# Performance work log

Measured on AMD Instinct MI355X. Metric: run time of the kernel, lower is better.

The kernel has to match this reference:

```python
import jax, jax.numpy as jnp
import numpy as np

B, C, H, W = 32, 256, 56, 56
HEADS, M, EXP = 8, 7, 4


def _rel_pos_index(m):
    # Swin V1 pair-wise relative position index, [m*m, m*m] (static)
    coords = np.stack(np.meshgrid(np.arange(m), np.arange(m), indexing='ij'))  # [2,m,m]
    cf = coords.reshape(2, -1)
    rel = (cf[:, :, None] - cf[:, None, :]).transpose(1, 2, 0).copy()
    rel[:, :, 0] += m - 1
    rel[:, :, 1] += m - 1
    rel[:, :, 0] *= 2 * m - 1
    return jnp.asarray(rel.sum(-1))


def setup_inputs():
    key = jax.random.key(0)
    ks = jax.random.split(key, 8)
    s = lambda k, shp: jax.random.normal(k, shp, jnp.float32) * 0.02
    return {
        'x': jax.random.normal(ks[0], (B, C, H, W), jnp.float32),
        'qkv_w': s(ks[1], (3 * C, C)), 'qkv_b': jnp.zeros((3 * C,), jnp.float32),
        'proj_w': s(ks[2], (C, C)), 'proj_b': jnp.zeros((C,), jnp.float32),
        'bias_table': s(ks[3], ((2 * M - 1) * (2 * M - 1), HEADS)),
        'ln1_g': jnp.ones((C,), jnp.float32), 'ln1_b': jnp.zeros((C,), jnp.float32),
        'ln2_g': jnp.ones((C,), jnp.float32), 'ln2_b': jnp.zeros((C,), jnp.float32),
        'w1': s(ks[4], (EXP * C, C)), 'b1': jnp.zeros((EXP * C,), jnp.float32),
        'w2': s(ks[5], (C, EXP * C)), 'b2': jnp.zeros((C,), jnp.float32),
    }


def _layernorm(x, g, b, eps=1e-5):
    mu = x.mean(-1, keepdims=True)
    var = ((x - mu) ** 2).mean(-1, keepdims=True)
    return (x - mu) * jax.lax.rsqrt(var + eps) * g + b


def _block(x, qkv_w, qkv_b, proj_w, proj_b, bias_table,
           ln1_g, ln1_b, ln2_g, ln2_b, w1, b1, w2, b2):
    Bx, Cx, Hx, Wx = x.shape
    N = M * M
    # window partition: [B,C,H,W] -> [B*nw, M*M, C]
    xp = x.reshape(Bx, Cx, Hx // M, M, Wx // M, M)
    xp = xp.transpose(0, 2, 4, 3, 5, 1).reshape(-1, N, Cx)
    B_ = xp.shape[0]
    # relative self-attention (pre-LN)
    h = _layernorm(xp, ln1_g, ln1_b)
    qkv = (h @ qkv_w.T + qkv_b).reshape(B_, N, 3, HEADS, Cx // HEADS)
    qkv = qkv.transpose(2, 0, 3, 1, 4)  # [3,B_,H,N,d]
    q, k, v = qkv[0], qkv[1], qkv[2]
    q = q * (HEADS ** -0.5)  # note: module scales by num_heads**-0.5 (faithful)
    rel_idx = _rel_pos_index(M)
    bias = bias_table[rel_idx.reshape(-1)].reshape(N, N, HEADS).transpose(2, 0, 1)
    attn = jax.nn.softmax(jnp.einsum('bhnd,bhmd->bhnm', q, k) + bias[None], axis=-1)
    out = jnp.einsum('bhnm,bhmd->bhnd', attn, v).transpose(0, 2, 1, 3).reshape(B_, N, Cx)
    xp = xp + (out @ proj_w.T + proj_b)
    # MLP (1x1 Conv1d == pointwise linear), exact GELU as in torch
    h2 = _layernorm(xp, ln2_g, ln2_b)
    h2 = jax.nn.gelu(h2 @ w1.T + b1, approximate=False)
    xp = xp + (h2 @ w2.T + b2)
    # window reverse: [B*nw, M*M, C] -> [B,C,H,W]
    nwh, nww = Hx // M, Wx // M
    y = xp.reshape(Bx, nwh, nww, M, M, Cx).transpose(0, 5, 1, 3, 2, 4).reshape(Bx, Cx, Hx, Wx)
    return y


def reference(x, qkv_w, qkv_b, proj_w, proj_b, bias_table,
              ln1_g, ln1_b, ln2_g, ln2_b, w1, b1, w2, b2):
    return _block(x, qkv_w, qkv_b, proj_w, proj_b, bias_table,
                  ln1_g, ln1_b, ln2_g, ln2_b, w1, b1, w2, b2)
```

## Files before the change

### kernel.cpp

```cpp
#include <hip/hip_runtime.h>
#include <math.h>

#define TB 256

typedef short bf16x8 __attribute__((ext_vector_type(8)));
typedef short s16x4 __attribute__((ext_vector_type(4)));
typedef float f32x4 __attribute__((ext_vector_type(4)));
typedef unsigned short u16;

__device__ __forceinline__ float b2f(u16 u){
  union{unsigned int i; float f;} v; v.i = ((unsigned int)u)<<16; return v.f;
}
__device__ __forceinline__ u16 f2b(float f){
  union{float ff; unsigned int i;} v; v.ff=f;
  return (u16)((v.i + 0x7FFFu + ((v.i>>16)&1u))>>16);
}

__global__ void k_cvt(const float* __restrict__ s, u16* __restrict__ d, int n){
  int i = blockIdx.x*TB + threadIdx.x;
  if(i<n) d[i] = f2b(s[i]);
}

__global__ void k_biasT(const float* __restrict__ table, float* __restrict__ out){
  int i = blockIdx.x*TB + threadIdx.x;
  if(i >= 8*64*64) return;
  int h = i>>12, kq = i&4095, k = kq>>6, q = kq&63;
  float v = 0.f;
  if(k<49 && q<49){
    int qi=q/7, qj=q-qi*7, ki=k/7, kj=k-ki*7;
    int idx = (qi-ki+6)*13 + (qj-kj+6);
    v = table[idx*8+h];
  }
  out[i] = v;
}

#define QB_OFF  32768
#define KB_OFF  65536
#define VT_OFF  98304
#define H2_OFF  65536
#define HID_OFF 98304
#define BLK_LDS 131072

__global__ __launch_bounds__(1024,1) void k_block(
    const float* __restrict__ x,
    const u16* __restrict__ wqkv,  const float* __restrict__ bqkv,
    const u16* __restrict__ wproj, const float* __restrict__ bproj,
    const float* __restrict__ biasT,
    const float* __restrict__ g1, const float* __restrict__ bt1,
    const u16* __restrict__ w1, const float* __restrict__ b1v,
    const u16* __restrict__ w2, const float* __restrict__ b2v,
    const float* __restrict__ g2, const float* __restrict__ bt2,
    float* __restrict__ xg)
{
  extern __shared__ char lds[];
  const int tid = threadIdx.x;
  const int wv = tid >> 6, l = tid & 63;
  const int lr = l & 15, lg = l >> 4;
  const unsigned swzA = ((unsigned)(lr & 7)) << 4;
  const unsigned swzR = ((unsigned)((lr>>2) & 3)) << 4;
  const int win = blockIdx.x;
  const int bb = win >> 6, wh = (win >> 3) & 7, ww = win & 7;
  const float* xwin = x + (size_t)bb*802816 + (size_t)wh*392 + ww*7;
  const size_t obase = (size_t)bb*802816 + (size_t)wh*392 + ww*7;

  {
    float gg[4], bgm[4];
    #pragma unroll
    for(int k2=0;k2<4;++k2){ gg[k2]=g1[l+64*k2]; bgm[k2]=bt1[l+64*k2]; }
    float xv[4][4];
    #pragma unroll
    for(int s=0;s<4;++s){
      int n = wv + s*16;
      if(n<49){
        int ii=n/7, jj=n-ii*7;
        const float* px = xwin + ii*56 + jj;
        #pragma unroll
        for(int k2=0;k2<4;++k2) xv[s][k2] = px[(size_t)(l+64*k2)*3136];
      }
    }
    #pragma unroll
    for(int s=0;s<4;++s){
      int n = wv + s*16;
      if(n<49){
        float sm=0.f, sq=0.f;
        #pragma unroll
        for(int k2=0;k2<4;++k2){ sm+=xv[s][k2]; sq+=xv[s][k2]*xv[s][k2]; }
        #pragma unroll
        for(int off=32;off>=1;off>>=1){ sm+=__shfl_xor(sm,off); sq+=__shfl_xor(sq,off); }
        float mu=sm*(1.f/256.f), var=sq*(1.f/256.f)-mu*mu;
        float rs=rsqrtf(var+1e-5f);
        #pragma unroll
        for(int k2=0;k2<4;++k2){
          int c=l+64*k2;
          unsigned off2 = (((unsigned)n)*512u + ((unsigned)c)*2u) ^ (((unsigned)(n&7))<<4);
          *(u16*)(lds + off2) = f2b((xv[s][k2]-mu)*rs*gg[k2]+bgm[k2]);
        }
      }
    }
  }
  for(int m=tid; m<3840; m+=1024) *(u16*)(lds + 49*512 + m*2) = 0;
  for(int m=tid; m<8192; m+=1024) *(unsigned*)(lds + VT_OFF + m*4) = 0u;
  __syncthreads();

  for(int ct=wv; ct<48; ct+=16){
    bf16x8 bfr[8];
    const u16* wrow = wqkv + ((size_t)(ct*16+lr))*256 + lg*8;
    #pragma unroll
    for(int k=0;k<8;++k) bfr[k] = *(const bf16x8*)(wrow + k*32);
    f32x4 b4 = *(const f32x4*)(bqkv + ct*16 + lg*4);
    const int s3 = ct>>4, hd = (ct>>1)&7, db = (ct&1)*16 + lg*4;
    #pragma unroll
    for(int rt=0; rt<4; ++rt){
      f32x4 acc = {0.f,0.f,0.f,0.f};
      #pragma unroll
      for(int k=0;k<8;++k){
        bf16x8 afr = *(const bf16x8*)(lds + ((((unsigned)(rt*16+lr))*512u + (unsigned)(k*64+lg*16)) ^ swzA));
        acc = __builtin_amdgcn_mfma_f32_16x16x32_bf16(bfr[k], afr, acc, 0,0,0);
      }
      const int r = rt*16 + lr;
      if(r<49){
        if(s3==0){
          s16x4 pk;
          #pragma unroll
          for(int i=0;i<4;++i) pk[i] = (short)f2b((acc[i]+b4[i])*0.35355339059327373f);
          *(s16x4*)(lds + ((unsigned)(QB_OFF + hd*4096 + r*64 + db*2) ^ swzR)) = pk;
        } else if(s3==1){
          s16x4 pk;
          #pragma unroll
          for(int i=0;i<4;++i) pk[i] = (short)f2b(acc[i]+b4[i]);
          *(s16x4*)(lds + ((unsigned)(KB_OFF + hd*4096 + r*64 + db*2) ^ swzR)) = pk;
        } else {
          #pragma unroll
          for(int i=0;i<4;++i)
            *(u16*)(lds + ((unsigned)(VT_OFF + hd*4096 + (db+i)*128 + r*2) ^ ((((unsigned)(db+i))&7u)<<4))) = f2b(acc[i]+b4[i]);
        }
      }
    }
  }
  __syncthreads();

  {
    const int h = wv & 7, half = wv >> 3;
    bf16x8 kf[4], qf[2];
    #pragma unroll
    for(int t=0;t<4;++t)
      kf[t] = *(const bf16x8*)(lds + ((unsigned)(KB_OFF + h*4096 + (t*16+lr)*64 + lg*16) ^ swzR));
    #pragma unroll
    for(int j=0;j<2;++j){
      int qt = half*2 + j;
      qf[j] = *(const bf16x8*)(lds + ((unsigned)(QB_OFF + h*4096 + (qt*16+lr)*64 + lg*16) ^ swzR));
    }
    f32x4 st[2][4];
    #pragma unroll
    for(int j=0;j<2;++j){
      const int qt = half*2 + j;
      #pragma unroll
      for(int kt=0;kt<4;++kt){
        f32x4 bini;
        #pragma unroll
        for(int i=0;i<4;++i) bini[i] = biasT[h*4096 + (kt*16+lg*4+i)*64 + qt*16+lr];
        st[j][kt] = __builtin_amdgcn_mfma_f32_16x16x32_bf16(kf[kt], qf[j], bini, 0,0,0);
      }
    }
    #pragma unroll
    for(int j=0;j<2;++j)
      #pragma unroll
      for(int i=0;i<4;++i)
        if(!(lg==0 && i==0)) st[j][3][i] = -1e30f;

    s16x4 pk[2][4];
    #pragma unroll
    for(int j=0;j<2;++j){
      float mx = -1e30f;
      #pragma unroll
      for(int kt=0;kt<4;++kt)
        #pragma unroll
        for(int i=0;i<4;++i) mx = fmaxf(mx, st[j][kt][i]);
      mx = fmaxf(mx, __shfl_xor(mx,16));
      mx = fmaxf(mx, __shfl_xor(mx,32));
      float su = 0.f;
      #pragma unroll
      for(int kt=0;kt<4;++kt)
        #pragma unroll
        for(int i=0;i<4;++i){ float p = __expf(st[j][kt][i]-mx); st[j][kt][i]=p; su+=p; }
      su += __shfl_xor(su,16);
      su += __shfl_xor(su,32);
      float inv = 1.f/su;
      #pragma unroll
      for(int kt=0;kt<4;++kt)
        #pragma unroll
        for(int i=0;i<4;++i) pk[j][kt][i] = (short)f2b(st[j][kt][i]*inv);
    }
    __syncthreads();

    char* Pb = lds + h*8192;
    #pragma unroll
    for(int j=0;j<2;++j){
      const unsigned rq = (unsigned)((half*2+j)*16 + lr);
      #pragma unroll
      for(int kt=0;kt<4;++kt)
        *(s16x4*)(Pb + ((rq*128u + (unsigned)(kt*32+lg*8)) ^ swzA)) = pk[j][kt];
    }
    bf16x8 pf[2][2], vf[2][2];
    #pragma unroll
    for(int j=0;j<2;++j){
      const unsigned rq = (unsigned)((half*2+j)*16 + lr);
      #pragma unroll
      for(int ks=0;ks<2;++ks)
        pf[j][ks] = *(const bf16x8*)(Pb + ((rq*128u + (unsigned)(ks*64+lg*16)) ^ swzA));
    }
    #pragma unroll
    for(int dt=0;dt<2;++dt)
      #pragma unroll
      for(int ks=0;ks<2;++ks)
        vf[dt][ks] = *(const bf16x8*)(lds + ((unsigned)(VT_OFF + h*4096 + (dt*16+lr)*128 + ks*64+lg*16) ^ swzA));
    #pragma unroll
    for(int j=0;j<2;++j){
      const int qt = half*2 + j;
      #pragma unroll
      for(int dt=0;dt<2;++dt){
        f32x4 o = {0.f,0.f,0.f,0.f};
        o = __builtin_amdgcn_mfma_f32_16x16x32_bf16(pf[j][0], vf[dt][0], o, 0,0,0);
        o = __builtin_amdgcn_mfma_f32_16x16x32_bf16(pf[j][1], vf[dt][1], o, 0,0,0);
        #pragma unroll
        for(int i=0;i<4;++i)
          *(u16*)(lds + ((unsigned)(KB_OFF + h*4096 + (qt*16+lg*4+i)*64 + (dt*16+lr)*2) ^ (((unsigned)lg)<<4))) = f2b(o[i]);
      }
    }
  }
  __syncthreads();

  float* xtf = (float*)lds;
  {
    const int c = wv*16 + lr;
    bf16x8 bfr[8];
    const u16* wrow = wproj + ((size_t)c)*256 + lg*8;
    #pragma unroll
    for(int k=0;k<8;++k) bfr[k] = *(const bf16x8*)(wrow + k*32);
    const float pb = bproj[c];
    #pragma unroll
    for(int mt=0; mt<4; ++mt){
      f32x4 acc = {0.f,0.f,0.f,0.f};
      #pragma unroll
      for(int ks=0;ks<8;++ks){
        bf16x8 afr = *(const bf16x8*)(lds + ((unsigned)(KB_OFF + ks*4096 + (mt*16+lr)*64 + lg*16) ^ swzR));
        acc = __builtin_amdgcn_mfma_f32_16x16x32_bf16(afr, bfr[ks], acc, 0,0,0);
      }
      #pragma unroll
      for(int i=0;i<4;++i){
        int r = mt*16 + lg*4 + i;
        if(r<49){
          int ii=r/7, jj=r-ii*7;
          xtf[r*256 + c] = acc[i] + pb + xwin[(size_t)c*3136 + ii*56 + jj];
        }
      }
    }
  }
  for(int m=tid; m<3840; m+=1024) xtf[49*256+m] = 0.f;
  __syncthreads();

  {
    float gg[4], bb2[4];
    #pragma unroll
    for(int k2=0;k2<4;++k2){ gg[k2]=g2[l+64*k2]; bb2[k2]=bt2[l+64*k2]; }
    #pragma unroll
    for(int rr=0; rr<4; ++rr){
      int r = wv*4 + rr;
      float v[4];
      #pragma unroll
      for(int k2=0;k2<4;++k2) v[k2]=xtf[r*256 + l + 64*k2];
      float sm=v[0]+v[1]+v[2]+v[3];
      float sq=v[0]*v[0]+v[1]*v[1]+v[2]*v[2]+v[3]*v[3];
      #pragma unroll
      for(int off=32;off>=1;off>>=1){ sm+=__shfl_xor(sm,off); sq+=__shfl_xor(sq,off); }
      float mu=sm*(1.f/256.f), var=sq*(1.f/256.f)-mu*mu, rs=rsqrtf(var+1e-5f);
      #pragma unroll
      for(int k2=0;k2<4;++k2){
        int c=l+64*k2;
        unsigned off2 = (unsigned)H2_OFF + ((((unsigned)r)*512u + ((unsigned)c)*2u) ^ (((unsigned)(r&7))<<4));
        *(u16*)(lds + off2) = f2b((v[k2]-mu)*rs*gg[k2]+bb2[k2]);
      }
    }
  }
  __syncthreads();

  f32x4 acc2[4];
  #pragma unroll
  for(int mt=0;mt<4;++mt) acc2[mt]=(f32x4){0.f,0.f,0.f,0.f};

  for(int kc=0; kc<4; ++kc){
    {
      const int hcol = wv*16 + lr;
      const int gcol = kc*256 + hcol;
      bf16x8 bfr[8];
      const u16* wrow = w1 + (size_t)gcol*256 + lg*8;
      #pragma unroll
      for(int k=0;k<8;++k) bfr[k]=*(const bf16x8*)(wrow + k*32);
      const float bias1 = b1v[gcol];
      #pragma unroll
      for(int mt=0; mt<4; ++mt){
        f32x4 acc={0.f,0.f,0.f,0.f};
        #pragma unroll
        for(int k=0;k<8;++k){
          bf16x8 afr = *(const bf16x8*)(lds + (unsigned)H2_OFF + ((((unsigned)(mt*16+lr))*512u + (unsigned)(k*64+lg*16)) ^ swzA));
          acc = __builtin_amdgcn_mfma_f32_16x16x32_bf16(afr, bfr[k], acc, 0,0,0);
        }
        #pragma unroll
        for(int i2=0;i2<4;++i2){
          int r = mt*16 + lg*4 + i2;
          float vv = acc[i2] + bias1;
          float gl = 0.5f*vv*(1.f + erff(vv*0.70710678118654752f));
          unsigned off2 = (unsigned)HID_OFF + ((((unsigned)r)*512u + ((unsigned)hcol)*2u) ^ (((unsigned)(r&7))<<4));
          *(u16*)(lds + off2) = f2b(gl);
        }
      }
    }
    __syncthreads();
    {
      const int c = wv*16 + lr;
      bf16x8 bfr[8];
      const u16* wrow = w2 + (size_t)c*1024 + kc*256 + lg*8;
      #pragma unroll
      for(int k=0;k<8;++k) bfr[k]=*(const bf16x8*)(wrow + k*32);
      #pragma unroll
      for(int mt=0; mt<4; ++mt){
        f32x4 a4 = acc2[mt];
        #pragma unroll
        for(int k=0;k<8;++k){
          bf16x8 afr = *(const bf16x8*)(lds + (unsigned)HID_OFF + ((((unsigned)(mt*16+lr))*512u + (unsigned)(k*64+lg*16)) ^ swzA));
          a4 = __builtin_amdgcn_mfma_f32_16x16x32_bf16(afr, bfr[k], a4, 0,0,0);
        }
        acc2[mt] = a4;
      }
    }
    __syncthreads();
  }

  {
    const int c = wv*16 + lr;
    const float biasc = b2v[c];
    #pragma unroll
    for(int mt=0; mt<4; ++mt){
      #pragma unroll
      for(int i2=0;i2<4;++i2){
        int r = mt*16 + lg*4 + i2;
        xtf[r*256 + c] = acc2[mt][i2] + biasc + xtf[r*256 + c];
      }
    }
  }
  __syncthreads();

  for(int u=tid; u<1792; u+=1024){
    int c = u/7, i = u - (u/7)*7;
    float* dst = xg + obase + (size_t)c*3136 + i*56;
    #pragma unroll
    for(int j=0;j<7;++j) dst[j] = xtf[(i*7+j)*256 + c];
  }
}

extern "C" void kernel_launch(void* const* d_in, const int* in_sizes, int n_in,
                              void* d_out, int out_size, void* d_ws, size_t ws_size,
                              hipStream_t stream) {
  const float* x      = (const float*)d_in[0];
  const float* qkv_w  = (const float*)d_in[1];
  const float* qkv_b  = (const float*)d_in[2];
  const float* proj_w = (const float*)d_in[3];
  const float* proj_b = (const float*)d_in[4];
  const float* btab   = (const float*)d_in[5];
  const float* ln1g   = (const float*)d_in[6];
  const float* ln1b   = (const float*)d_in[7];
  const float* ln2g   = (const float*)d_in[8];
  const float* ln2b   = (const float*)d_in[9];
  const float* w1     = (const float*)d_in[10];
  const float* b1     = (const float*)d_in[11];
  const float* w2     = (const float*)d_in[12];
  const float* b2     = (const float*)d_in[13];

  char* ws = (char*)d_ws;
  float* biasT = (float*)ws;
  u16*   wq    = (u16*)(ws + 131072);
  u16*   wp    = (u16*)(ws + 524288);
  u16*   w1b   = (u16*)(ws + 655360);
  u16*   w2b   = (u16*)(ws + 1179648);

  k_cvt<<<196608/TB, TB, 0, stream>>>(qkv_w, wq, 196608);
  k_cvt<<<65536/TB,  TB, 0, stream>>>(proj_w, wp, 65536);
  k_cvt<<<262144/TB, TB, 0, stream>>>(w1, w1b, 262144);
  k_cvt<<<262144/TB, TB, 0, stream>>>(w2, w2b, 262144);
  k_biasT<<<32768/TB, TB, 0, stream>>>(btab, biasT);

  hipFuncSetAttribute((const void*)k_block, hipFuncAttributeMaxDynamicSharedMemorySize, BLK_LDS);
  k_block<<<2048, 1024, BLK_LDS, stream>>>(x, wq, qkv_b, wp, proj_b, biasT, ln1g, ln1b,
                                           w1b, b1, w2b, b2, ln2g, ln2b, (float*)d_out);
}
```

Baseline: 878.0 us.

## Double-buffer MLP hidden tile, prefetch weights, bf16 residual, fuse prep kernels

The five weight-conversion and bias-table launches are merged into one prep kernel. In the main kernel, block indices are remapped across windows, and the projection and first MLP weights are loaded into registers before the preceding barriers. The MLP hidden tile is double-buffered in LDS so that each chunk's fc1+GELU overlaps the previous chunk's fc2, which halves the number of barriers. Also: exact erff is replaced with a polynomial erf approximation, the residual is kept as bf16 in LDS, and the fc2 MFMA loop runs at raised wave priority. These reduce synchronisation stalls and launch overhead, at the cost of residual precision and higher register pressure.

```diff
diff --git a/kernel.cpp b/kernel.cpp
--- a/kernel.cpp
+++ b/kernel.cpp
@@ -9,36 +9,51 @@
 typedef unsigned short u16;
 
 __device__ __forceinline__ float b2f(u16 u){
-  union{unsigned int i; float f;} v; v.i = ((unsigned int)u)<<16; return v.f;
+  union{unsigned i; float f;} v; v.i=((unsigned)u)<<16; return v.f;
 }
 __device__ __forceinline__ u16 f2b(float f){
-  union{float ff; unsigned int i;} v; v.ff=f;
+  union{float ff; unsigned i;} v; v.ff=f;
   return (u16)((v.i + 0x7FFFu + ((v.i>>16)&1u))>>16);
 }
 
-__global__ void k_cvt(const float* __restrict__ s, u16* __restrict__ d, int n){
+__device__ __forceinline__ float gelu(float x){
+  float z = fabsf(x)*0.70710678118654752f;
+  float t = 1.0f/fmaf(0.3275911f, z, 1.0f);
+  float p = t*fmaf(t, fmaf(t, fmaf(t, fmaf(t, 1.061405429f, -1.453152027f), 1.421413741f), -0.284496736f), 0.254829592f);
+  float erfz = fmaf(-p, __expf(-z*z), 1.0f);
+  float s = (x >= 0.f) ? erfz : -erfz;
+  return 0.5f*x*(1.0f + s);
+}
+
+__global__ void k_prep(const float* __restrict__ qkv_w, const float* __restrict__ proj_w,
+                       const float* __restrict__ w1, const float* __restrict__ w2,
+                       const float* __restrict__ btab,
+                       u16* __restrict__ wq, u16* __restrict__ wp,
+                       u16* __restrict__ w1b, u16* __restrict__ w2b,
+                       float* __restrict__ biasT){
   int i = blockIdx.x*TB + threadIdx.x;
-  if(i<n) d[i] = f2b(s[i]);
-}
-
-__global__ void k_biasT(const float* __restrict__ table, float* __restrict__ out){
-  int i = blockIdx.x*TB + threadIdx.x;
-  if(i >= 8*64*64) return;
-  int h = i>>12, kq = i&4095, k = kq>>6, q = kq&63;
-  float v = 0.f;
-  if(k<49 && q<49){
-    int qi=q/7, qj=q-qi*7, ki=k/7, kj=k-ki*7;
-    int idx = (qi-ki+6)*13 + (qj-kj+6);
-    v = table[idx*8+h];
-  }
-  out[i] = v;
+  if(i < 196608){ wq[i] = f2b(qkv_w[i]); return; }
+  i -= 196608;
+  if(i < 65536){ wp[i] = f2b(proj_w[i]); return; }
+  i -= 65536;
+  if(i < 262144){ w1b[i] = f2b(w1[i]); return; }
+  i -= 262144;
+  if(i < 262144){ w2b[i] = f2b(w2[i]); return; }
+  i -= 262144;
+  if(i < 32768){
+    int h = i>>12, kq = i&4095, k = kq>>6, q = kq&63;
+    float v = 0.f;
+    if(k<49 && q<49){
+      int qi=q/7, qj=q-qi*7, ki=k/7, kj=k-ki*7;
+      v = btab[((qi-ki+6)*13 + (qj-kj+6))*8 + h];
+    }
+    biasT[i] = v;
+  }
 }
 
 #define QB_OFF  32768
 #define KB_OFF  65536
 #define VT_OFF  98304
-#define H2_OFF  65536
-#define HID_OFF 98304
 #define BLK_LDS 131072
 
 __global__ __launch_bounds__(1024,1) void k_block(
@@ -58,7 +73,7 @@
   const int lr = l & 15, lg = l >> 4;
   const unsigned swzA = ((unsigned)(lr & 7)) << 4;
   const unsigned swzR = ((unsigned)((lr>>2) & 3)) << 4;
-  const int win = blockIdx.x;
+  const int win = ((blockIdx.x & 7) << 8) | (blockIdx.x >> 3);
   const int bb = win >> 6, wh = (win >> 3) & 7, ww = win & 7;
   const float* xwin = x + (size_t)bb*802816 + (size_t)wh*392 + ww*7;
   const size_t obase = (size_t)bb*802816 + (size_t)wh*392 + ww*7;
@@ -137,6 +152,15 @@
       }
     }
   }
+  bf16x8 bfrP[8];
+  float pbP;
+  {
+    const int c = wv*16 + lr;
+    const u16* wrow = wproj + (size_t)c*256 + lg*8;
+    #pragma unroll
+    for(int k=0;k<8;++k) bfrP[k] = *(const bf16x8*)(wrow + k*32);
+    pbP = bproj[c];
+  }
   __syncthreads();
 
   {
@@ -168,7 +192,7 @@
       for(int i=0;i<4;++i)
         if(!(lg==0 && i==0)) st[j][3][i] = -1e30f;
 
-    s16x4 pk[2][4];
+    s16x4 pkk[2][4];
     #pragma unroll
     for(int j=0;j<2;++j){
       float mx = -1e30f;
@@ -189,7 +213,7 @@
       #pragma unroll
       for(int kt=0;kt<4;++kt)
         #pragma unroll
-        for(int i=0;i<4;++i) pk[j][kt][i] = (short)f2b(st[j][kt][i]*inv);
+        for(int i=0;i<4;++i) pkk[j][kt][i] = (short)f2b(st[j][kt][i]*inv);
     }
     __syncthreads();
 
@@ -199,7 +223,7 @@
       const unsigned rq = (unsigned)((half*2+j)*16 + lr);
       #pragma unroll
       for(int kt=0;kt<4;++kt)
-        *(s16x4*)(Pb + ((rq*128u + (unsigned)(kt*32+lg*8)) ^ swzA)) = pk[j][kt];
+        *(s16x4*)(Pb + ((rq*128u + (unsigned)(kt*32+lg*8)) ^ swzA)) = pkk[j][kt];
     }
     bf16x8 pf[2][2], vf[2][2];
     #pragma unroll
@@ -230,33 +254,40 @@
   }
   __syncthreads();
 
-  float* xtf = (float*)lds;
   {
     const int c = wv*16 + lr;
-    bf16x8 bfr[8];
-    const u16* wrow = wproj + ((size_t)c)*256 + lg*8;
-    #pragma unroll
-    for(int k=0;k<8;++k) bfr[k] = *(const bf16x8*)(wrow + k*32);
-    const float pb = bproj[c];
     #pragma unroll
     for(int mt=0; mt<4; ++mt){
       f32x4 acc = {0.f,0.f,0.f,0.f};
       #pragma unroll
       for(int ks=0;ks<8;++ks){
         bf16x8 afr = *(const bf16x8*)(lds + ((unsigned)(KB_OFF + ks*4096 + (mt*16+lr)*64 + lg*16) ^ swzR));
-        acc = __builtin_amdgcn_mfma_f32_16x16x32_bf16(afr, bfr[ks], acc, 0,0,0);
+        acc = __builtin_amdgcn_mfma_f32_16x16x32_bf16(afr, bfrP[ks], acc, 0,0,0);
       }
       #pragma unroll
       for(int i=0;i<4;++i){
         int r = mt*16 + lg*4 + i;
         if(r<49){
           int ii=r/7, jj=r-ii*7;
-          xtf[r*256 + c] = acc[i] + pb + xwin[(size_t)c*3136 + ii*56 + jj];
-        }
-      }
-    }
-  }
-  for(int m=tid; m<3840; m+=1024) xtf[49*256+m] = 0.f;
+          float val = acc[i] + pbP + xwin[(size_t)c*3136 + ii*56 + jj];
+          *(u16*)(lds + ((((unsigned)r)*512u + ((unsigned)c)*2u) ^ (((unsigned)(r&7))<<4))) = f2b(val);
+        }
+      }
+    }
+  }
+  for(int m=tid; m<3840; m+=1024){
+    int r = 49 + (m>>8), c = m & 255;
+    *(u16*)(lds + ((((unsigned)r)*512u + ((unsigned)c)*2u) ^ (((unsigned)(r&7))<<4))) = 0;
+  }
+  bf16x8 bfr1[8];
+  float bias1;
+  {
+    const int gcol = wv*16 + lr;
+    const u16* wrow = w1 + (size_t)gcol*256 + lg*8;
+    #pragma unroll
+    for(int k=0;k<8;++k) bfr1[k] = *(const bf16x8*)(wrow + k*32);
+    bias1 = b1v[gcol];
+  }
   __syncthreads();
 
   {
@@ -268,7 +299,8 @@
       int r = wv*4 + rr;
       float v[4];
       #pragma unroll
-      for(int k2=0;k2<4;++k2) v[k2]=xtf[r*256 + l + 64*k2];
+      for(int k2=0;k2<4;++k2)
+        v[k2] = b2f(*(const u16*)(lds + ((((unsigned)r)*512u + ((unsigned)(l+64*k2))*2u) ^ (((unsigned)(r&7))<<4))));
       float sm=v[0]+v[1]+v[2]+v[3];
       float sq=v[0]*v[0]+v[1]*v[1]+v[2]*v[2]+v[3]*v[3];
       #pragma unroll
@@ -277,74 +309,94 @@
       #pragma unroll
       for(int k2=0;k2<4;++k2){
         int c=l+64*k2;
-        unsigned off2 = (unsigned)H2_OFF + ((((unsigned)r)*512u + ((unsigned)c)*2u) ^ (((unsigned)(r&7))<<4));
+        unsigned off2 = 32768u + ((((unsigned)r)*512u + ((unsigned)c)*2u) ^ (((unsigned)(r&7))<<4));
         *(u16*)(lds + off2) = f2b((v[k2]-mu)*rs*gg[k2]+bb2[k2]);
       }
     }
   }
   __syncthreads();
 
+  const int hcol = wv*16 + lr;
+  const unsigned hid_off[2] = {98304u, 65536u};
   f32x4 acc2[4];
   #pragma unroll
   for(int mt=0;mt<4;++mt) acc2[mt]=(f32x4){0.f,0.f,0.f,0.f};
 
+  #pragma unroll
+  for(int mt=0; mt<4; ++mt){
+    f32x4 acc={0.f,0.f,0.f,0.f};
+    #pragma unroll
+    for(int k=0;k<8;++k){
+      bf16x8 afr = *(const bf16x8*)(lds + 32768u + ((((unsigned)(mt*16+lr))*512u + (unsigned)(k*64+lg*16)) ^ swzA));
+      acc = __builtin_amdgcn_mfma_f32_16x16x32_bf16(afr, bfr1[k], acc, 0,0,0);
+    }
+    #pragma unroll
+    for(int i2=0;i2<4;++i2){
+      int r = mt*16 + lg*4 + i2;
+      *(u16*)(lds + hid_off[0] + ((((unsigned)r)*512u + ((unsigned)hcol)*2u) ^ (((unsigned)(r&7))<<4))) = f2b(gelu(acc[i2]+bias1));
+    }
+  }
+  __syncthreads();
+
   for(int kc=0; kc<4; ++kc){
-    {
-      const int hcol = wv*16 + lr;
-      const int gcol = kc*256 + hcol;
-      bf16x8 bfr[8];
+    bf16x8 bfrN[8]; float biasN = 0.f;
+    if(kc<3){
+      const int gcol = (kc+1)*256 + hcol;
       const u16* wrow = w1 + (size_t)gcol*256 + lg*8;
       #pragma unroll
-      for(int k=0;k<8;++k) bfr[k]=*(const bf16x8*)(wrow + k*32);
-      const float bias1 = b1v[gcol];
+      for(int k=0;k<8;++k) bfrN[k] = *(const bf16x8*)(wrow + k*32);
+      biasN = b1v[gcol];
+    }
+    if(kc<3){
+      const unsigned dst = hid_off[(kc+1)&1];
       #pragma unroll
       for(int mt=0; mt<4; ++mt){
         f32x4 acc={0.f,0.f,0.f,0.f};
         #pragma unroll
         for(int k=0;k<8;++k){
-          bf16x8 afr = *(const bf16x8*)(lds + (unsigned)H2_OFF + ((((unsigned)(mt*16+lr))*512u + (unsigned)(k*64+lg*16)) ^ swzA));
-          acc = __builtin_amdgcn_mfma_f32_16x16x32_bf16(afr, bfr[k], acc, 0,0,0);
+          bf16x8 afr = *(const bf16x8*)(lds + 32768u + ((((unsigned)(mt*16+lr))*512u + (unsigned)(k*64+lg*16)) ^ swzA));
+          acc = __builtin_amdgcn_mfma_f32_16x16x32_bf16(afr, bfrN[k], acc, 0,0,0);
         }
         #pragma unroll
         for(int i2=0;i2<4;++i2){
           int r = mt*16 + lg*4 + i2;
-          float vv = acc[i2] + bias1;
-          float gl = 0.5f*vv*(1.f + erff(vv*0.70710678118654752f));
-          unsigned off2 = (unsigned)HID_OFF + ((((unsigned)r)*512u + ((unsigned)hcol)*2u) ^ (((unsigned)(r&7))<<4));
-          *(u16*)(lds + off2) = f2b(gl);
-        }
-      }
-    }
-    __syncthreads();
+          *(u16*)(lds + dst + ((((unsigned)r)*512u + ((unsigned)hcol)*2u) ^ (((unsigned)(r&7))<<4))) = f2b(gelu(acc[i2]+biasN));
+        }
+      }
+    }
     {
-      const int c = wv*16 + lr;
-      bf16x8 bfr[8];
-      const u16* wrow = w2 + (size_t)c*1024 + kc*256 + lg*8;
-      #pragma unroll
-      for(int k=0;k<8;++k) bfr[k]=*(const bf16x8*)(wrow + k*32);
+      bf16x8 bfr2[8];
+      const u16* wrow = w2 + (size_t)hcol*1024 + kc*256 + lg*8;
+      #pragma unroll
+      for(int k=0;k<8;++k) bfr2[k] = *(const bf16x8*)(wrow + k*32);
+      const unsigned src = hid_off[kc&1];
+      __builtin_amdgcn_s_setprio(1);
       #pragma unroll
       for(int mt=0; mt<4; ++mt){
         f32x4 a4 = acc2[mt];
         #pragma unroll
         for(int k=0;k<8;++k){
-          bf16x8 afr = *(const bf16x8*)(lds + (unsigned)HID_OFF + ((((unsigned)(mt*16+lr))*512u + (unsigned)(k*64+lg*16)) ^ swzA));
-          a4 = __builtin_amdgcn_mfma_f32_16x16x32_bf16(afr, bfr[k], a4, 0,0,0);
+          bf16x8 afr = *(const bf16x8*)(lds + src + ((((unsigned)(mt*16+lr))*512u + (unsigned)(k*64+lg*16)) ^ swzA));
+          a4 = __builtin_amdgcn_mfma_f32_16x16x32_bf16(afr, bfr2[k], a4, 0,0,0);
         }
         acc2[mt] = a4;
       }
+      __builtin_amdgcn_s_setprio(0);
     }
     __syncthreads();
   }
 
   {
-    const int c = wv*16 + lr;
+    const int c = hcol;
     const float biasc = b2v[c];
     #pragma unroll
     for(int mt=0; mt<4; ++mt){
       #pragma unroll
       for(int i2=0;i2<4;++i2){
         int r = mt*16 + lg*4 + i2;
-        xtf[r*256 + c] = acc2[mt][i2] + biasc + xtf[r*256 + c];
+        float resid = b2f(*(const u16*)(lds + ((((unsigned)r)*512u + ((unsigned)c)*2u) ^ (((unsigned)(r&7))<<4))));
+        float val = acc2[mt][i2] + biasc + resid;
+        *(float*)(lds + 32768u + ((((unsigned)r)*1024u + ((unsigned)c)*4u) ^ ((((unsigned)(r>>2))&3u)<<6))) = val;
       }
     }
   }
@@ -354,7 +406,10 @@
     int c = u/7, i = u - (u/7)*7;
     float* dst = xg + obase + (size_t)c*3136 + i*56;
     #pragma unroll
-    for(int j=0;j<7;++j) dst[j] = xtf[(i*7+j)*256 + c];
+    for(int j=0;j<7;++j){
+      int r = i*7+j;
+      dst[j] = *(const float*)(lds + 32768u + ((((unsigned)r)*1024u + ((unsigned)c)*4u) ^ ((((unsigned)(r>>2))&3u)<<6)));
+    }
   }
 }
 
@@ -383,11 +438,7 @@
   u16*   w1b   = (u16*)(ws + 655360);
   u16*   w2b   = (u16*)(ws + 1179648);
 
-  k_cvt<<<196608/TB, TB, 0, stream>>>(qkv_w, wq, 196608);
-  k_cvt<<<65536/TB,  TB, 0, stream>>>(proj_w, wp, 65536);
-  k_cvt<<<262144/TB, TB, 0, stream>>>(w1, w1b, 262144);
-  k_cvt<<<262144/TB, TB, 0, stream>>>(w2, w2b, 262144);
-  k_biasT<<<32768/TB, TB, 0, stream>>>(btab, biasT);
+  k_prep<<<3200, TB, 0, stream>>>(qkv_w, proj_w, w1, w2, btab, wq, wp, w1b, w2b, biasT);
 
   hipFuncSetAttribute((const void*)k_block, hipFuncAttributeMaxDynamicSharedMemorySize, BLK_LDS);
   k_block<<<2048, 1024, BLK_LDS, stream>>>(x, wq, qkv_b, wp, proj_b, biasT, ln1g, ln1b,
```

Result: slower. 1.105 ms (+25.8%).
